# Performance work log

Hardware: AMD Instinct MI355X
Metric: run time of the kernel (lower is better)

The kernel has to match this reference:

```python
import jax, jax.numpy as jnp
import numpy as np

B, T, C = 8, 2048, 1024
HEAD = 64

def setup_inputs() -> dict:
    key = jax.random.key(0)
    k1, k2, k3, k4 = jax.random.split(key, 4)
    x = jax.random.normal(k1, (B, T, C), dtype=jnp.float32)
    # nn.Linear(n_embed, head_size, bias=False): y = x @ W^T; store as [C, HEAD] for x @ W
    scale = 1.0 / np.sqrt(C)
    Wq = jax.random.normal(k2, (C, HEAD), dtype=jnp.float32) * scale
    Wk = jax.random.normal(k3, (C, HEAD), dtype=jnp.float32) * scale
    Wv = jax.random.normal(k4, (C, HEAD), dtype=jnp.float32) * scale
    return {"x": x, "Wq": Wq, "Wk": Wk, "Wv": Wv}

def reference(x, Wq, Wk, Wv):
    Bx, Tx, Cx = x.shape
    q = x @ Wq            # [B,T,H]
    k = x @ Wk            # [B,T,H]
    v = x @ Wv            # [B,T,H]
    # NOTE: original scales by C**-0.5 (embedding dim), not head_size**-0.5
    aff = jnp.einsum('bqh,bkh->bqk', q, k) * (Cx ** -0.5)  # [B,T,T]
    causal = jnp.tril(jnp.ones((Tx, Tx), dtype=bool))
    aff = jnp.where(causal, aff, -jnp.inf)
    probs = jax.nn.softmax(aff, axis=-1)
    # dropout p=0.0 (eval): identity
    return jnp.einsum('bqk,bkh->bqh', probs, v)
```

## Files before the change

### kernel.cpp

```cpp
#include <hip/hip_runtime.h>
#include <hip/hip_bf16.h>

typedef __attribute__((ext_vector_type(8))) short bf16x8;
typedef __attribute__((ext_vector_type(4))) float f32x4;
typedef __attribute__((ext_vector_type(4))) int i32x4;

#define LOG2E 1.4426950408889634f

static __device__ __forceinline__ unsigned int f2bfu(float f) {
    return (unsigned int)__builtin_bit_cast(unsigned short, __float2bfloat16(f));
}
static __device__ __forceinline__ unsigned int pack2(float lo, float hi) {
    return (f2bfu(hi) << 16) | f2bfu(lo);
}
static __device__ __forceinline__ unsigned short f2bf(float f) {
    return __builtin_bit_cast(unsigned short, __float2bfloat16(f));
}
static __device__ __forceinline__ void gload16(const void* g, void* l) {
    __builtin_amdgcn_global_load_lds(
        (const __attribute__((address_space(1))) unsigned int*)g,
        (__attribute__((address_space(3))) unsigned int*)l,
        16, 0, 0);
}

__global__ __launch_bounds__(256) void wtrans_kernel(
    const float* __restrict__ Wq, const float* __restrict__ Wk,
    const float* __restrict__ Wv, unsigned short* __restrict__ Wts)
{
    const int part = blockIdx.x;
    const int t    = blockIdx.y;
    const int c    = part * 256 + threadIdx.x;
    const int n    = c >> 3;
    const int mat  = n >> 6;
    const int nl   = n & 63;
    const int k0   = t * 64 + (c & 7) * 8;
    const float* W = (mat == 0) ? Wq : ((mat == 1) ? Wk : Wv);
    const float scale = (mat == 0) ? 0.03125f : 1.0f;
    unsigned int s[8];
#pragma unroll
    for (int j = 0; j < 8; ++j)
        s[j] = (unsigned int)f2bf(W[(size_t)(k0 + j) * 64 + nl] * scale);
    i32x4 pk;
    pk[0] = (int)(s[0] | (s[1] << 16));
    pk[1] = (int)(s[2] | (s[3] << 16));
    pk[2] = (int)(s[4] | (s[5] << 16));
    pk[3] = (int)(s[6] | (s[7] << 16));
    *(i32x4*)(Wts + (size_t)t * 12288 + (size_t)c * 8) = pk;
}

__global__ __launch_bounds__(256, 4) void proj_kernel(
    const float* __restrict__ x, const unsigned short* __restrict__ Wts,
    unsigned short* __restrict__ Qb, unsigned short* __restrict__ Kp,
    unsigned short* __restrict__ Vp)
{
    __shared__ __align__(16) unsigned short sA[2][32][72];
    __shared__ __align__(16) unsigned short sBlin[12288];

    const int tid  = threadIdx.x;
    const int w    = tid >> 6;
    const int wm   = w >> 1;
    const int wn   = w & 1;
    const int lane = tid & 63;
    const int r    = lane & 15;
    const int g    = lane >> 4;
    const int xv   = r & 7;
    const int mbase = blockIdx.x * 32;

    const int arow = tid >> 3;
    const int acb  = (tid & 7) * 8;
    const float* xptr = x + (size_t)(mbase + arow) * 1024 + acb;

    f32x4 acc[6];
#pragma unroll
    for (int i = 0; i < 6; ++i) acc[i] = (f32x4)0.0f;

    float4 XAa0, XAa1, XAb0, XAb1;

#define LOADX(S0, S1, t_) do { \
        const float* xp = xptr + (size_t)(t_) * 64; \
        S0 = *(const float4*)(xp);  S1 = *(const float4*)(xp + 4); \
    } while (0)

#define GLOADB(t_) do { \
        const unsigned short* wtb = Wts + (size_t)(t_) * 12288; \
        _Pragma("unroll") \
        for (int i = 0; i < 6; ++i) { \
            const int sslot = (w * 6 + i) * 64 + lane; \
            const int ssrc  = sslot ^ ((sslot >> 3) & 7); \
            gload16(wtb + (size_t)ssrc * 8, &sBlin[(size_t)(w * 6 + i) * 512]); \
        } \
    } while (0)

#define STOREA(buf, S0, S1) do { \
        i32x4 pa0 = {(int)pack2(S0.x, S0.y), (int)pack2(S0.z, S0.w), \
                     (int)pack2(S1.x, S1.y), (int)pack2(S1.z, S1.w)}; \
        *(i32x4*)&sA[buf][arow][acb] = pa0; \
    } while (0)

#define COMPSTEP(buf) do { \
        _Pragma("unroll") \
        for (int h = 0; h < 2; ++h) { \
            bf16x8 af = *(const bf16x8*)&sA[buf][wm * 16 + r][h * 32 + g * 8]; \
            _Pragma("unroll") \
            for (int nt = 0; nt < 6; ++nt) { \
                bf16x8 bfr = *(const bf16x8*)&sBlin[ \
                    (size_t)((nt * 2 + wn) * 16 + r) * 64 + (((h * 4 + g) ^ xv) << 3)]; \
                acc[nt] = __builtin_amdgcn_mfma_f32_16x16x32_bf16(af, bfr, acc[nt], 0, 0, 0); \
            } \
        } \
    } while (0)

    GLOADB(0);
    LOADX(XAa0, XAa1, 0);
    LOADX(XAb0, XAb1, 1);
#pragma unroll 1
    for (int t = 0; t < 16; t += 2) {
        STOREA(0, XAa0, XAa1);
        __syncthreads();
        if (t + 2 < 16) LOADX(XAa0, XAa1, t + 2);
        COMPSTEP(0);
        __syncthreads();
        GLOADB(t + 1);

        STOREA(1, XAb0, XAb1);
        __syncthreads();
        if (t + 3 < 16) LOADX(XAb0, XAb1, t + 3);
        COMPSTEP(1);
        __syncthreads();
        if (t + 2 < 16) GLOADB(t + 2);
    }

    unsigned short (*sK)[72]  = (unsigned short (*)[72])&sBlin[0];
    unsigned short (*sVT)[48] = (unsigned short (*)[48])&sBlin[2560];
    const int row0  = mbase + wm * 16 + g * 4;
    const int lrow0 = wm * 16 + g * 4;
#pragma unroll
    for (int nt = 0; nt < 6; ++nt) {
        const int ti  = nt * 2 + wn;
        const int mat = ti >> 2;
        const int col = (ti & 3) * 16 + r;
#pragma unroll
        for (int j = 0; j < 4; ++j) {
            const float v = acc[nt][j];
            if (mat == 0) {
                Qb[(size_t)(row0 + j) * 64 + col] = f2bf(v);
            } else if (mat == 1) {
                sK[lrow0 + j][col] = f2bf(v);
            } else {
                sVT[col][lrow0 + j] = f2bf(v);
            }
        }
    }
    __syncthreads();
    {
        const int bb = mbase >> 11;
        const int tt = (mbase & 2047) >> 5;
        const int f  = tid >> 6;
        const int r2 = lane & 15, g2 = lane >> 4;
        const int krow = 8 * (r2 >> 2) + (r2 & 3) + (f >> 1) * 4;
        const int kcol = (f & 1) * 32 + g2 * 8;
        *(i32x4*)(Kp + ((size_t)(bb * 64 + tt) * 4 + f) * 512 + lane * 8)
            = *(const i32x4*)&sK[krow][kcol];
        *(i32x4*)(Vp + ((size_t)(bb * 64 + tt) * 4 + f) * 512 + lane * 8)
            = *(const i32x4*)&sVT[f * 16 + r2][g2 * 8];
    }
}

__global__ __launch_bounds__(512, 2) void attn_kernel(
    const unsigned short* __restrict__ Qb, const unsigned short* __restrict__ Kp,
    const unsigned short* __restrict__ Vp, float* __restrict__ out)
{
    __shared__ __align__(16) float sO[8][2][4][64][4];
    __shared__ float sM[8][2][16], sL[8][2][16];

    const int tid  = threadIdx.x;
    const int w    = tid >> 6;
    const int lane = tid & 63;
    const int r    = lane & 15;
    const int g    = lane >> 4;
    const int b    = blockIdx.x & 7;
    const int p    = blockIdx.x >> 3;
    const int qbL  = p * 32;
    const int qbH  = 2016 - p * 32;
    const int lastqL = qbL + 31;
    const int lastqH = qbH + 31;

    const unsigned short* Qbb = Qb + (size_t)b * 2048 * 64;
    const unsigned short* Kpb = Kp + (size_t)b * 64 * 2048;
    const unsigned short* Vpb = Vp + (size_t)b * 64 * 2048;

#define QBASE(qs) ((qs) < 2 ? (qbL + (qs) * 16) : (qbH + ((qs) - 2) * 16))

    bf16x8 qf[4][2];
#pragma unroll
    for (int qs = 0; qs < 4; ++qs)
#pragma unroll
        for (int h = 0; h < 2; ++h)
            qf[qs][h] = *(const bf16x8*)(Qbb + (size_t)(QBASE(qs) + r) * 64 + h * 32 + g * 8);

    f32x4 o[4][4];
#pragma unroll
    for (int qs = 0; qs < 4; ++qs)
#pragma unroll
        for (int i = 0; i < 4; ++i) o[qs][i] = (f32x4)0.0f;
    float m[4] = {-1e30f, -1e30f, -1e30f, -1e30f};
    float l[4] = {0.0f, 0.0f, 0.0f, 0.0f};

#define LOADK(K_, kvt) do { \
        const unsigned short* kp = Kpb + (size_t)(kvt) * 2048 + lane * 8; \
        K_[0] = *(const bf16x8*)(kp); \
        K_[1] = *(const bf16x8*)(kp + 512); \
        K_[2] = *(const bf16x8*)(kp + 1024); \
        K_[3] = *(const bf16x8*)(kp + 1536); \
    } while (0)
#define LOADV(V_, kvt) do { \
        const unsigned short* vp = Vpb + (size_t)(kvt) * 2048 + lane * 8; \
        _Pragma("unroll") \
        for (int i = 0; i < 4; ++i) V_[i] = *(const bf16x8*)(vp + i * 512); \
    } while (0)

    bf16x8 KA[4], VA[4];
#pragma unroll 1
    for (int kv0 = w * 32; kv0 <= lastqH; kv0 += 256) {
        const bool doLow = (kv0 <= lastqL);

        LOADK(KA, kv0 >> 5);
        LOADV(VA, kv0 >> 5);

        f32x4 s0[4], s1[4];
        __builtin_amdgcn_s_setprio(1);
#pragma unroll
        for (int qs = 0; qs < 4; ++qs) {
            s0[qs] = (f32x4)0.0f; s1[qs] = (f32x4)0.0f;
            if (qs < 2 && !doLow) continue;
            s0[qs] = __builtin_amdgcn_mfma_f32_16x16x32_bf16(KA[0], qf[qs][0], s0[qs], 0, 0, 0);
            s0[qs] = __builtin_amdgcn_mfma_f32_16x16x32_bf16(KA[1], qf[qs][1], s0[qs], 0, 0, 0);
            s1[qs] = __builtin_amdgcn_mfma_f32_16x16x32_bf16(KA[2], qf[qs][0], s1[qs], 0, 0, 0);
            s1[qs] = __builtin_amdgcn_mfma_f32_16x16x32_bf16(KA[3], qf[qs][1], s1[qs], 0, 0, 0);
        }
        __builtin_amdgcn_s_setprio(0);

        float lm[4] = {-1e30f, -1e30f, -1e30f, -1e30f};
#pragma unroll
        for (int qs = 0; qs < 4; ++qs) {
            if (qs < 2 && !doLow) continue;
            const int q = QBASE(qs) + r;
            if (kv0 + 31 > QBASE(qs)) {
#pragma unroll
                for (int j = 0; j < 4; ++j) {
                    if (kv0 + 8 * g + j > q)     s0[qs][j] = -1e30f;
                    if (kv0 + 8 * g + 4 + j > q) s1[qs][j] = -1e30f;
                }
            }
            lm[qs] = fmaxf(fmaxf(fmaxf(s0[qs][0], s0[qs][1]), fmaxf(s0[qs][2], s0[qs][3])),
                           fmaxf(fmaxf(s1[qs][0], s1[qs][1]), fmaxf(s1[qs][2], s1[qs][3])));
        }
        if (!__all(lm[0] <= m[0] + 8.0f && lm[1] <= m[1] + 8.0f &&
                   lm[2] <= m[2] + 8.0f && lm[3] <= m[3] + 8.0f)) {
#pragma unroll
            for (int qs = 0; qs < 4; ++qs) {
                float t2 = fmaxf(lm[qs], __shfl_xor(lm[qs], 16));
                t2 = fmaxf(t2, __shfl_xor(t2, 32));
                const float mn = fmaxf(m[qs], t2);
                const float alpha = __builtin_amdgcn_exp2f((m[qs] - mn) * LOG2E);
#pragma unroll
                for (int ht = 0; ht < 4; ++ht) o[qs][ht] *= alpha;
                l[qs] *= alpha;
                m[qs] = mn;
            }
        }

        __builtin_amdgcn_s_setprio(1);
#pragma unroll
        for (int qs = 0; qs < 4; ++qs) {
            if (qs < 2 && !doLow) continue;
            float p0[4], p1[4];
#pragma unroll
            for (int j = 0; j < 4; ++j) {
                p0[j] = __builtin_amdgcn_exp2f((s0[qs][j] - m[qs]) * LOG2E);
                p1[j] = __builtin_amdgcn_exp2f((s1[qs][j] - m[qs]) * LOG2E);
                l[qs] += p0[j] + p1[j];
            }
            i32x4 pw;
            pw[0] = (int)pack2(p0[0], p0[1]);
            pw[1] = (int)pack2(p0[2], p0[3]);
            pw[2] = (int)pack2(p1[0], p1[1]);
            pw[3] = (int)pack2(p1[2], p1[3]);
            bf16x8 pfrag = __builtin_bit_cast(bf16x8, pw);
            o[qs][0] = __builtin_amdgcn_mfma_f32_16x16x32_bf16(VA[0], pfrag, o[qs][0], 0, 0, 0);
            o[qs][1] = __builtin_amdgcn_mfma_f32_16x16x32_bf16(VA[1], pfrag, o[qs][1], 0, 0, 0);
            o[qs][2] = __builtin_amdgcn_mfma_f32_16x16x32_bf16(VA[2], pfrag, o[qs][2], 0, 0, 0);
            o[qs][3] = __builtin_amdgcn_mfma_f32_16x16x32_bf16(VA[3], pfrag, o[qs][3], 0, 0, 0);
        }
        __builtin_amdgcn_s_setprio(0);
    }

#define MERGE_STORE(QS, Q2) do { \
        float lr = l[QS]; \
        lr += __shfl_xor(lr, 16); \
        lr += __shfl_xor(lr, 32); \
        if (g == 0) { sM[w][Q2][r] = m[QS]; sL[w][Q2][r] = lr; } \
        _Pragma("unroll") \
        for (int ht = 0; ht < 4; ++ht) *(f32x4*)&sO[w][Q2][ht][lane][0] = o[QS][ht]; \
    } while (0)

#define MERGE_WRITE(QBASE0) do { \
        const int q2 = w >> 2, ht = w & 3; \
        float M = sM[0][q2][r]; \
        _Pragma("unroll") \
        for (int wp = 1; wp < 8; ++wp) M = fmaxf(M, sM[wp][q2][r]); \
        float L = 0.0f; \
        float beta[8]; \
        _Pragma("unroll") \
        for (int wp = 0; wp < 8; ++wp) { \
            beta[wp] = __builtin_amdgcn_exp2f((sM[wp][q2][r] - M) * LOG2E); \
            L += beta[wp] * sL[wp][q2][r]; \
        } \
        f32x4 av = (f32x4)0.0f; \
        _Pragma("unroll") \
        for (int wp = 0; wp < 8; ++wp) { \
            f32x4 t = *(const f32x4*)&sO[wp][q2][ht][lane][0]; \
            av += t * beta[wp]; \
        } \
        const float inv = 1.0f / L; \
        const int qrow = (QBASE0) + q2 * 16 + r; \
        *(f32x4*)(out + ((size_t)b * 2048 + qrow) * 64 + ht * 16 + g * 4) = av * inv; \
    } while (0)

    MERGE_STORE(0, 0);
    MERGE_STORE(1, 1);
    __syncthreads();
    MERGE_WRITE(qbL);
    __syncthreads();
    MERGE_STORE(2, 0);
    MERGE_STORE(3, 1);
    __syncthreads();
    MERGE_WRITE(qbH);
}

extern "C" void kernel_launch(void* const* d_in, const int* in_sizes, int n_in,
                              void* d_out, int out_size, void* d_ws, size_t ws_size,
                              hipStream_t stream) {
    const float* x  = (const float*)d_in[0];
    const float* Wq = (const float*)d_in[1];
    const float* Wk = (const float*)d_in[2];
    const float* Wv = (const float*)d_in[3];
    float* out = (float*)d_out;

    unsigned short* Qb  = (unsigned short*)d_ws;
    unsigned short* Kp  = Qb + (size_t)8 * 2048 * 64;
    unsigned short* Vp  = Kp + (size_t)8 * 64 * 2048;
    unsigned short* Wts = Vp + (size_t)8 * 64 * 2048;

    hipLaunchKernelGGL(wtrans_kernel, dim3(6, 16), dim3(256), 0, stream, Wq, Wk, Wv, Wts);
    hipLaunchKernelGGL(proj_kernel, dim3(512), dim3(256), 0, stream, x, Wts, Qb, Kp, Vp);
    hipLaunchKernelGGL(attn_kernel, dim3(256), dim3(512), 0, stream, Qb, Kp, Vp, out);
}
```

Before: 42.91 us.

## Halve projection row tile to 16 rows and double grid size

The projection kernel now processes 16 rows of x per block instead of 32, launching 1024 blocks rather than 512. Each wave handles all 16 rows for 3 of the 12 output column tiles, and the K/V packing epilogue writes only the half of each 32-row packed tile that the block owns. This gives more blocks to fill the 256 CUs. The cost is that each block reloads the full weight matrix into LDS for half as many rows, which doubles weight traffic and cuts MFMA reuse per B fragment.

```diff
diff --git a/kernel.cpp b/kernel.cpp
--- a/kernel.cpp
+++ b/kernel.cpp
@@ -53,33 +53,28 @@
     unsigned short* __restrict__ Qb, unsigned short* __restrict__ Kp,
     unsigned short* __restrict__ Vp)
 {
-    __shared__ __align__(16) unsigned short sA[2][32][72];
+    __shared__ __align__(16) unsigned short sA[2][16][72];
     __shared__ __align__(16) unsigned short sBlin[12288];
 
     const int tid  = threadIdx.x;
     const int w    = tid >> 6;
-    const int wm   = w >> 1;
-    const int wn   = w & 1;
     const int lane = tid & 63;
     const int r    = lane & 15;
     const int g    = lane >> 4;
     const int xv   = r & 7;
-    const int mbase = blockIdx.x * 32;
-
-    const int arow = tid >> 3;
-    const int acb  = (tid & 7) * 8;
+    const int mbase = blockIdx.x * 16;
+
+    const int arow = tid >> 4;
+    const int acb  = (tid & 15) * 4;
     const float* xptr = x + (size_t)(mbase + arow) * 1024 + acb;
 
-    f32x4 acc[6];
-#pragma unroll
-    for (int i = 0; i < 6; ++i) acc[i] = (f32x4)0.0f;
-
-    float4 XAa0, XAa1, XAb0, XAb1;
-
-#define LOADX(S0, S1, t_) do { \
-        const float* xp = xptr + (size_t)(t_) * 64; \
-        S0 = *(const float4*)(xp);  S1 = *(const float4*)(xp + 4); \
-    } while (0)
+    f32x4 acc[3];
+#pragma unroll
+    for (int i = 0; i < 3; ++i) acc[i] = (f32x4)0.0f;
+
+    float4 Xa, Xb;
+
+#define LOADX(S, t_) do { S = *(const float4*)(xptr + (size_t)(t_) * 64); } while (0)
 
 #define GLOADB(t_) do { \
         const unsigned short* wtb = Wts + (size_t)(t_) * 12288; \
@@ -91,78 +86,77 @@
         } \
     } while (0)
 
-#define STOREA(buf, S0, S1) do { \
-        i32x4 pa0 = {(int)pack2(S0.x, S0.y), (int)pack2(S0.z, S0.w), \
-                     (int)pack2(S1.x, S1.y), (int)pack2(S1.z, S1.w)}; \
-        *(i32x4*)&sA[buf][arow][acb] = pa0; \
+#define STOREA(buf, S) do { \
+        unsigned long long pa = ((unsigned long long)pack2(S.z, S.w) << 32) \
+                              | (unsigned long long)pack2(S.x, S.y); \
+        *(unsigned long long*)&sA[buf][arow][acb] = pa; \
     } while (0)
 
 #define COMPSTEP(buf) do { \
         _Pragma("unroll") \
         for (int h = 0; h < 2; ++h) { \
-            bf16x8 af = *(const bf16x8*)&sA[buf][wm * 16 + r][h * 32 + g * 8]; \
+            bf16x8 af = *(const bf16x8*)&sA[buf][r][h * 32 + g * 8]; \
             _Pragma("unroll") \
-            for (int nt = 0; nt < 6; ++nt) { \
+            for (int nt = 0; nt < 3; ++nt) { \
                 bf16x8 bfr = *(const bf16x8*)&sBlin[ \
-                    (size_t)((nt * 2 + wn) * 16 + r) * 64 + (((h * 4 + g) ^ xv) << 3)]; \
+                    (size_t)((nt * 4 + w) * 16 + r) * 64 + (((h * 4 + g) ^ xv) << 3)]; \
                 acc[nt] = __builtin_amdgcn_mfma_f32_16x16x32_bf16(af, bfr, acc[nt], 0, 0, 0); \
             } \
         } \
     } while (0)
 
     GLOADB(0);
-    LOADX(XAa0, XAa1, 0);
-    LOADX(XAb0, XAb1, 1);
+    LOADX(Xa, 0);
+    LOADX(Xb, 1);
 #pragma unroll 1
     for (int t = 0; t < 16; t += 2) {
-        STOREA(0, XAa0, XAa1);
+        STOREA(0, Xa);
         __syncthreads();
-        if (t + 2 < 16) LOADX(XAa0, XAa1, t + 2);
+        if (t + 2 < 16) LOADX(Xa, t + 2);
         COMPSTEP(0);
         __syncthreads();
         GLOADB(t + 1);
 
-        STOREA(1, XAb0, XAb1);
+        STOREA(1, Xb);
         __syncthreads();
-        if (t + 3 < 16) LOADX(XAb0, XAb1, t + 3);
+        if (t + 3 < 16) LOADX(Xb, t + 3);
         COMPSTEP(1);
         __syncthreads();
         if (t + 2 < 16) GLOADB(t + 2);
     }
 
     unsigned short (*sK)[72]  = (unsigned short (*)[72])&sBlin[0];
-    unsigned short (*sVT)[48] = (unsigned short (*)[48])&sBlin[2560];
-    const int row0  = mbase + wm * 16 + g * 4;
-    const int lrow0 = wm * 16 + g * 4;
-#pragma unroll
-    for (int nt = 0; nt < 6; ++nt) {
-        const int ti  = nt * 2 + wn;
-        const int mat = ti >> 2;
-        const int col = (ti & 3) * 16 + r;
-#pragma unroll
-        for (int j = 0; j < 4; ++j) {
-            const float v = acc[nt][j];
-            if (mat == 0) {
-                Qb[(size_t)(row0 + j) * 64 + col] = f2bf(v);
-            } else if (mat == 1) {
-                sK[lrow0 + j][col] = f2bf(v);
-            } else {
-                sVT[col][lrow0 + j] = f2bf(v);
-            }
-        }
+    unsigned short (*sVT)[24] = (unsigned short (*)[24])&sBlin[1152];
+    const int colw = w * 16 + r;
+#pragma unroll
+    for (int j = 0; j < 4; ++j) {
+        const int lrow = g * 4 + j;
+        Qb[(size_t)(mbase + lrow) * 64 + colw] = f2bf(acc[0][j]);
+    }
+    __syncthreads();
+#pragma unroll
+    for (int j = 0; j < 4; ++j) {
+        const int lrow = g * 4 + j;
+        sK[lrow][colw]  = f2bf(acc[1][j]);
+        sVT[colw][lrow] = f2bf(acc[2][j]);
     }
     __syncthreads();
     {
-        const int bb = mbase >> 11;
-        const int tt = (mbase & 2047) >> 5;
-        const int f  = tid >> 6;
+        const int bb   = mbase >> 11;
+        const int tt   = (mbase & 2047) >> 5;
+        const int half = (mbase >> 4) & 1;
+        const int f    = tid >> 6;
         const int r2 = lane & 15, g2 = lane >> 4;
-        const int krow = 8 * (r2 >> 2) + (r2 & 3) + (f >> 1) * 4;
-        const int kcol = (f & 1) * 32 + g2 * 8;
-        *(i32x4*)(Kp + ((size_t)(bb * 64 + tt) * 4 + f) * 512 + lane * 8)
-            = *(const i32x4*)&sK[krow][kcol];
-        *(i32x4*)(Vp + ((size_t)(bb * 64 + tt) * 4 + f) * 512 + lane * 8)
-            = *(const i32x4*)&sVT[f * 16 + r2][g2 * 8];
+        if (((r2 >> 3) & 1) == half) {
+            const int krow = (8 * (r2 >> 2) + (r2 & 3) + (f >> 1) * 4) & 15;
+            const int kcol = (f & 1) * 32 + g2 * 8;
+            *(i32x4*)(Kp + ((size_t)(bb * 64 + tt) * 4 + f) * 512 + lane * 8)
+                = *(const i32x4*)&sK[krow][kcol];
+        }
+        if (((g2 >> 1) & 1) == half) {
+            *(i32x4*)(Vp + ((size_t)(bb * 64 + tt) * 4 + f) * 512 + lane * 8)
+                = *(const i32x4*)&sVT[f * 16 + r2][(g2 & 1) * 8];
+        }
     }
 }
 
@@ -353,6 +347,6 @@
     unsigned short* Wts = Vp + (size_t)8 * 64 * 2048;
 
     hipLaunchKernelGGL(wtrans_kernel, dim3(6, 16), dim3(256), 0, stream, Wq, Wk, Wv, Wts);
-    hipLaunchKernelGGL(proj_kernel, dim3(512), dim3(256), 0, stream, x, Wts, Qb, Kp, Vp);
+    hipLaunchKernelGGL(proj_kernel, dim3(1024), dim3(256), 0, stream, x, Wts, Qb, Kp, Vp);
     hipLaunchKernelGGL(attn_kernel, dim3(256), dim3(512), 0, stream, Qb, Kp, Vp, out);
 }
```

New measurement: 46.92 us. 1.09x slower.
